# Optimization experiments

Hardware: AMD Instinct MI355X
Metric: run time of the kernel (lower is better)

The kernel has to match this reference:

```python
import jax, jax.numpy as jnp
import numpy as np

NUM_NODES = 15000


def _gcn_conv(x, W, b, src, dst, norm, num_nodes):
    # PyG GCNConv: x' = D^-1/2 (A + I) D^-1/2 (x W) + b
    h = x @ W                                   # [N, out]
    msg = h[src] * norm[:, None]                # gather + scale per edge
    out = jax.ops.segment_sum(msg, dst, num_segments=num_nodes)
    return out + b


def setup_inputs() -> dict:
    key = jax.random.key(0)
    ks = jax.random.split(key, 12)
    T = 100000
    E = 200000
    inp = {
        "x": jax.random.normal(ks[0], (NUM_NODES, 768), jnp.float32),
        "r_emb": jax.random.normal(ks[1], (T, 768), jnp.float32),
        "W1": jax.random.normal(ks[2], (768, 10), jnp.float32) * 0.05,
        "b1": jax.random.normal(ks[3], (10,), jnp.float32) * 0.05,
        "W2": jax.random.normal(ks[4], (10, 128), jnp.float32) * 0.05,
        "b2": jax.random.normal(ks[5], (128,), jnp.float32) * 0.05,
        "W_ih": jax.random.normal(ks[6], (512, 1024), jnp.float32) * 0.03,
        "W_hh": jax.random.normal(ks[7], (512, 128), jnp.float32) * 0.03,
        "b_ih": jax.random.normal(ks[8], (512,), jnp.float32) * 0.03,
        "b_hh": jax.random.normal(ks[9], (512,), jnp.float32) * 0.03,
        "edge_index": jax.random.randint(ks[10], (2, E), 0, NUM_NODES).astype(jnp.int64),
        "triples": jax.random.randint(ks[11], (T, 3), 0, NUM_NODES).astype(jnp.int64),
    }
    return inp


def reference(x, r_emb, W1, b1, W2, b2, W_ih, W_hh, b_ih, b_hh, edge_index, triples):
    N = x.shape[0]
    H = 128  # lstm hidden size
    # --- add self loops, symmetric GCN normalization ---
    loop = jnp.arange(N, dtype=edge_index.dtype)
    src = jnp.concatenate([edge_index[0], loop])
    dst = jnp.concatenate([edge_index[1], loop])
    deg = jax.ops.segment_sum(jnp.ones_like(dst, jnp.float32), dst, num_segments=N)
    dinv = jnp.where(deg > 0, jax.lax.rsqrt(deg), 0.0)
    norm = dinv[src] * dinv[dst]                      # [E+N]
    # --- 2-layer GCN ---
    h = jax.nn.relu(_gcn_conv(x, W1, b1, src, dst, norm, N))   # [N, 10]
    z = _gcn_conv(h, W2, b2, src, dst, norm, N)                # [N, 128]
    # --- per-triple LSTM scoring, batched (seq_len=1, zero init state) ---
    hvec = z[triples[:, 0]]                           # [T, 128]
    tvec = z[triples[:, 2]]                           # [T, 128]
    feat = jnp.concatenate([hvec, r_emb, tvec], axis=-1)       # [T, 1024]
    gates = feat @ W_ih.T + (b_ih + b_hh)             # [T, 512]; h0=0 so W_hh term vanishes
    i_g, f_g, g_g, o_g = jnp.split(gates, 4, axis=-1)  # torch gate order i,f,g,o
    c = jax.nn.sigmoid(i_g) * jnp.tanh(g_g)           # c0 = 0 -> forget term drops
    out = jax.nn.sigmoid(o_g) * jnp.tanh(c)           # [T, 128]
    score = jax.nn.sigmoid(jnp.sum(out, axis=-1))     # [T]
    return score
```

## Files before the change

kernel.cpp:

```cpp
#include <hip/hip_runtime.h>

#define NF 768
#define D1 10
#define D2 128
#define BM 64

typedef __attribute__((ext_vector_type(8))) short bf16x8;
typedef __attribute__((ext_vector_type(16))) float f32x16;

static __device__ __forceinline__ float sigf(float v){ return 1.0f/(1.0f+__expf(-v)); }
static __device__ __forceinline__ float tanhfast(float v){ return 2.0f/(1.0f+__expf(-2.0f*v)) - 1.0f; }
static __device__ __forceinline__ short f2bf(float f){
    unsigned u = __float_as_uint(f);
    u += 0x7fffu + ((u>>16)&1u);
    return (short)(u>>16);
}

static __device__ __forceinline__ void gload16(const void* g, void* l){
    __builtin_amdgcn_global_load_lds(
        (const __attribute__((address_space(1))) unsigned int*)(unsigned long long)g,
        (__attribute__((address_space(3))) unsigned int*)(unsigned long long)l,
        16, 0, 0);
}

static __device__ __forceinline__ short4 cvt4(float4 a){
    unsigned u0,u1;
    asm("v_cvt_pk_bf16_f32 %0, %1, %2" : "=v"(u0) : "v"(a.x), "v"(a.y));
    asm("v_cvt_pk_bf16_f32 %0, %1, %2" : "=v"(u1) : "v"(a.z), "v"(a.w));
    union { unsigned u[2]; short4 s; } r;
    r.u[0]=u0; r.u[1]=u1;
    return r.s;
}

__global__ void k_deg(const int* __restrict__ dst, int* __restrict__ cnt, int E){
    int e = blockIdx.x*256 + threadIdx.x;
    if(e<E) atomicAdd(&cnt[dst[e]], 1);
}

__global__ __launch_bounds__(256) void k_scan(const int* __restrict__ cnt,
                                              int* __restrict__ rowptr, int* __restrict__ rowcur,
                                              float* __restrict__ dinv, int N, int E){
    __shared__ int part[256];
    int t = threadIdx.x;
    int C = (N+255)/256;
    int lo = t*C, hi = lo+C; if(hi>N) hi=N; if(lo>N) lo=N;
    int s=0;
    for(int i=lo;i<hi;i++) s += cnt[i];
    part[t]=s;
    __syncthreads();
    if(t==0){
        int run=0;
        for(int i=0;i<256;i++){ int v=part[i]; part[i]=run; run+=v; }
        rowptr[N]=E;
    }
    __syncthreads();
    int run = part[t];
    for(int i=lo;i<hi;i++){
        rowptr[i]=run; rowcur[i]=run; run += cnt[i];
        dinv[i] = rsqrtf((float)cnt[i] + 1.0f);
    }
}

__global__ void k_fill(const int* __restrict__ src, const int* __restrict__ dst,
                       const float* __restrict__ dinv, int* __restrict__ rowcur,
                       int* __restrict__ esrc, float* __restrict__ enorm, int E){
    int e = blockIdx.x*256 + threadIdx.x;
    if(e>=E) return;
    int s=src[e], d=dst[e];
    int pos = atomicAdd(&rowcur[d], 1);
    esrc[pos]=s;
    enorm[pos]=dinv[s]*dinv[d];
}

__global__ __launch_bounds__(256) void k_h1(const float* __restrict__ x,
                                            const float* __restrict__ W1,
                                            float* __restrict__ h1, int N){
    __shared__ float wt[D1*NF];
    for(int idx=threadIdx.x; idx<NF*D1; idx+=256){
        int k=idx/D1, c=idx-k*D1;
        wt[c*NF+k]=W1[idx];
    }
    __syncthreads();
    int row = blockIdx.x*4 + (threadIdx.x>>6);
    int lane = threadIdx.x&63;
    if(row>=N) return;
    const float4* xr = (const float4*)(x + (size_t)row*NF);
    float acc[D1];
#pragma unroll
    for(int c=0;c<D1;c++) acc[c]=0.f;
#pragma unroll
    for(int i=0;i<3;i++){
        float4 v = xr[lane + 64*i];
#pragma unroll
        for(int c=0;c<D1;c++){
            float4 w = *(const float4*)&wt[c*NF + (lane+64*i)*4];
            acc[c] += v.x*w.x + v.y*w.y + v.z*w.z + v.w*w.w;
        }
    }
#pragma unroll
    for(int c=0;c<D1;c++){
        float v=acc[c];
#pragma unroll
        for(int off=32;off;off>>=1) v += __shfl_down(v,off,64);
        acc[c]=v;
    }
    if(lane==0){
#pragma unroll
        for(int c=0;c<D1;c++) h1[(size_t)row*D1+c]=acc[c];
    }
}

__global__ __launch_bounds__(128) void k_gh(const float* __restrict__ h1,
        const int* __restrict__ rowptr, const int* __restrict__ esrc,
        const float* __restrict__ enorm, const float* __restrict__ dinv,
        const float* __restrict__ b1, const float* __restrict__ W2,
        float* __restrict__ hz, int N){
    __shared__ float w2s[D1*D2];
    int tid = threadIdx.x;
    for(int i=tid;i<D1*D2;i+=128) w2s[i]=W2[i];
    __syncthreads();
    int node = blockIdx.x*2 + (tid>>6);
    int lane = tid&63;
    if(node>=N) return;
    int e0=rowptr[node], e1=rowptr[node+1];
    float acc[D1];
#pragma unroll
    for(int c=0;c<D1;c++) acc[c]=0.f;
    for(int e=e0+lane; e<e1; e+=64){
        int s=esrc[e]; float w=enorm[e];
        const float* hr = h1 + (size_t)s*D1;
#pragma unroll
        for(int c=0;c<D1;c++) acc[c] += hr[c]*w;
    }
#pragma unroll
    for(int c=0;c<D1;c++){
        float v=acc[c];
#pragma unroll
        for(int off=32;off;off>>=1) v += __shfl_down(v,off,64);
        acc[c] = __shfl(v, 0, 64);
    }
    float di=dinv[node], d2=di*di;
    const float* hr = h1 + (size_t)node*D1;
    float h[D1];
#pragma unroll
    for(int c=0;c<D1;c++){
        float v = acc[c] + hr[c]*d2 + b1[c];
        h[c] = v>0.f ? v : 0.f;
    }
    float o0=0.f, o1=0.f;
#pragma unroll
    for(int k=0;k<D1;k++){
        o0 += h[k]*w2s[k*D2 + lane];
        o1 += h[k]*w2s[k*D2 + 64 + lane];
    }
    hz[(size_t)node*D2 + lane]      = o0;
    hz[(size_t)node*D2 + 64 + lane] = o1;
}

__global__ __launch_bounds__(128) void k_gath2(const float* __restrict__ hz,
        const int* __restrict__ rowptr, const int* __restrict__ esrc,
        const float* __restrict__ enorm, const float* __restrict__ dinv,
        const float* __restrict__ b2, float* __restrict__ zbf, int N){
    int n = blockIdx.x;
    int c = threadIdx.x;
    int e0 = rowptr[n], e1 = rowptr[n+1];
    float di = dinv[n];
    float acc = hz[(size_t)n*D2+c]*di*di + b2[c];
    int e = e0;
    for(; e+1<e1; e+=2){
        int s0=esrc[e], s1=esrc[e+1];
        float w0=enorm[e], w1=enorm[e+1];
        acc += hz[(size_t)s0*D2+c]*w0 + hz[(size_t)s1*D2+c]*w1;
    }
    if(e<e1) acc += hz[(size_t)esrc[e]*D2+c]*enorm[e];
    zbf[(size_t)n*D2+c] = acc;
}

__global__ void k_wimgB(const float* __restrict__ Wih, ushort* __restrict__ img,
                        int* __restrict__ cnt, int N){
    int gid = blockIdx.x*256 + threadIdx.x;
    if(gid < N) cnt[gid] = 0;
    if(gid >= 12*64*64) return;
    int l = gid & 63;
    int ks16 = (gid>>6) & 63;
    int f = gid >> 12;
    int dd = l & 31, kb = l>>5;
    int wn = f/3, gi = f - wn*3;
    int gbase = (gi==0)?0:((gi==1)?256:384);
    int wrow = gbase + wn*32 + dd;
    int k = ks16*16 + kb*8;
    const float* p = Wih + (size_t)wrow*1024 + k;
    float4 v0=*(const float4*)p, v1=*(const float4*)(p+4);
    ushort o[8];
    o[0]=f2bf(v0.x); o[1]=f2bf(v0.y); o[2]=f2bf(v0.z); o[3]=f2bf(v0.w);
    o[4]=f2bf(v1.x); o[5]=f2bf(v1.y); o[6]=f2bf(v1.z); o[7]=f2bf(v1.w);
    *(int4*)(img + (size_t)gid*8) = *(int4*)o;
}

__global__ __launch_bounds__(256,3) void k_big(
    const float* __restrict__ remb, const ushort* __restrict__ img,
    const float* __restrict__ zbf, const float* __restrict__ b_ih,
    const float* __restrict__ b_hh, const int* __restrict__ trip,
    float* __restrict__ rowacc, int T)
{
    __shared__ ushort Ab[2][2*64*8];
    __shared__ ushort Br[3][12*512];
    int tid=threadIdx.x, lane=tid&63, w=tid>>6;
    int l31=lane&31, lh=lane>>5;
    int t0=blockIdx.x*BM;

    const int arow = w*16 + (lane>>2);
    const int asub = lane&3;
    int tc = t0 + arow; if(tc>=T) tc=T-1;
    const float* pzh = zbf + (size_t)trip[3*tc]*D2   + asub*4;
    const float* prm = remb + (size_t)tc*NF          + asub*4;
    const float* pzt = zbf + (size_t)trip[3*tc+2]*D2 + asub*4;
    const int awoff = ((asub>>1)*64 + arow)*8 + (asub&1)*4;
    const int ar0 = (lh*64 + l31)*8;
    const int ar1 = (lh*64 + 32 + l31)*8;

    f32x16 acc[2][3];
    const f32x16 zer = {0,0,0,0,0,0,0,0,0,0,0,0,0,0,0,0};
#pragma unroll
    for(int m=0;m<2;m++)
#pragma unroll
        for(int g=0;g<3;g++) acc[m][g]=zer;

    float4 pa[4];

#define ALOAD(C_) if((C_)<64){ \
    const float* s_; \
    if((C_)<8)       s_ = pzh + (C_)*16; \
    else if((C_)<56) s_ = prm + ((C_)-8)*16; \
    else             s_ = pzt + ((C_)-56)*16; \
    pa[(C_)&3] = *(const float4*)s_; }

#define AWRITE(C_) if((C_)<64){ \
    *(short4*)&Ab[(C_)&1][awoff] = cvt4(pa[(C_)&3]); }

#define BISSUE(C_) if((C_)<64){ \
    _Pragma("unroll") \
    for(int j_=0;j_<3;j_++){ \
        gload16(img + ((size_t)((w*3+j_)*64 + (C_))*64 + lane)*8, \
                &Br[(C_)%3][(w*3+j_)*512]); \
    } }

#define CH(C_,W_) { \
    asm volatile("s_waitcnt vmcnt(" W_ ")" ::: "memory"); \
    __builtin_amdgcn_sched_barrier(0); \
    asm volatile("s_waitcnt lgkmcnt(0)" ::: "memory"); \
    __builtin_amdgcn_s_barrier(); \
    __builtin_amdgcn_sched_barrier(0); \
    BISSUE((C_)+2) \
    __builtin_amdgcn_sched_barrier(0); \
    ALOAD((C_)+4) \
    __builtin_amdgcn_sched_barrier(0); \
    { \
        const ushort* a_ = &Ab[(C_)&1][0]; \
        const ushort* b_ = &Br[(C_)%3][0]; \
        bf16x8 A0_ = *(const bf16x8*)&a_[ar0]; \
        bf16x8 A1_ = *(const bf16x8*)&a_[ar1]; \
        bf16x8 B0_ = *(const bf16x8*)&b_[((w*3+0)*64+lane)*8]; \
        bf16x8 B1_ = *(const bf16x8*)&b_[((w*3+1)*64+lane)*8]; \
        bf16x8 B2_ = *(const bf16x8*)&b_[((w*3+2)*64+lane)*8]; \
        __builtin_amdgcn_s_setprio(1); \
        acc[0][0]=__builtin_amdgcn_mfma_f32_32x32x16_bf16(A0_,B0_,acc[0][0],0,0,0); \
        acc[0][1]=__builtin_amdgcn_mfma_f32_32x32x16_bf16(A0_,B1_,acc[0][1],0,0,0); \
        acc[0][2]=__builtin_amdgcn_mfma_f32_32x32x16_bf16(A0_,B2_,acc[0][2],0,0,0); \
        acc[1][0]=__builtin_amdgcn_mfma_f32_32x32x16_bf16(A1_,B0_,acc[1][0],0,0,0); \
        acc[1][1]=__builtin_amdgcn_mfma_f32_32x32x16_bf16(A1_,B1_,acc[1][1],0,0,0); \
        acc[1][2]=__builtin_amdgcn_mfma_f32_32x32x16_bf16(A1_,B2_,acc[1][2],0,0,0); \
        __builtin_amdgcn_s_setprio(0); \
    } \
    AWRITE((C_)+1) \
}

    ALOAD(0) ALOAD(1) ALOAD(2) ALOAD(3)
    __builtin_amdgcn_sched_barrier(0);
    BISSUE(0) BISSUE(1)
    __builtin_amdgcn_sched_barrier(0);
    AWRITE(0)

    CH(0 ,"3") CH(1 ,"4") CH(2 ,"5") CH(3 ,"5") CH(4 ,"5") CH(5 ,"5") CH(6 ,"5") CH(7 ,"5")
    CH(8 ,"5") CH(9 ,"5") CH(10,"5") CH(11,"5") CH(12,"5") CH(13,"5") CH(14,"5") CH(15,"5")
    CH(16,"5") CH(17,"5") CH(18,"5") CH(19,"5") CH(20,"5") CH(21,"5") CH(22,"5") CH(23,"5")
    CH(24,"5") CH(25,"5") CH(26,"5") CH(27,"5") CH(28,"5") CH(29,"5") CH(30,"5") CH(31,"5")
    CH(32,"5") CH(33,"5") CH(34,"5") CH(35,"5") CH(36,"5") CH(37,"5") CH(38,"5") CH(39,"5")
    CH(40,"5") CH(41,"5") CH(42,"5") CH(43,"5") CH(44,"5") CH(45,"5") CH(46,"5") CH(47,"5")
    CH(48,"5") CH(49,"5") CH(50,"5") CH(51,"5") CH(52,"5") CH(53,"5") CH(54,"5") CH(55,"5")
    CH(56,"5") CH(57,"5") CH(58,"5") CH(59,"5") CH(60,"5") CH(61,"4") CH(62,"3") CH(63,"0")
#undef CH
#undef BISSUE
#undef AWRITE
#undef ALOAD

    int d = w*32+l31;
    float bi=b_ih[d]+b_hh[d];
    float bg=b_ih[256+d]+b_hh[256+d];
    float bo=b_ih[384+d]+b_hh[384+d];
#pragma unroll
    for(int m=0;m<2;m++){
#pragma unroll
        for(int r=0;r<16;r++){
            int row = m*32 + (r&3)+8*(r>>2)+4*lh;
            int t = t0+row;
            float ov = 0.f;
            if(t<T){
                float ig = acc[m][0][r] + bi;
                float gg = acc[m][1][r] + bg;
                float og = acc[m][2][r] + bo;
                float cc = sigf(ig)*tanhfast(gg);
                ov = sigf(og)*tanhfast(cc);
            }
#pragma unroll
            for(int off=1; off<32; off<<=1) ov += __shfl_xor(ov, off, 64);
            if(l31==0 && t<T) atomicAdd(&rowacc[t], ov);
        }
    }
}

__global__ void k_sig(const float* __restrict__ rowacc, float* __restrict__ score, int T){
    int t = blockIdx.x*256 + threadIdx.x;
    if(t<T) score[t] = sigf(rowacc[t]);
}

extern "C" void kernel_launch(void* const* d_in, const int* in_sizes, int n_in,
                              void* d_out, int out_size, void* d_ws, size_t ws_size,
                              hipStream_t stream){
    const float* x    = (const float*)d_in[0];
    const float* remb = (const float*)d_in[1];
    const float* W1   = (const float*)d_in[2];
    const float* b1   = (const float*)d_in[3];
    const float* W2   = (const float*)d_in[4];
    const float* b2   = (const float*)d_in[5];
    const float* Wih  = (const float*)d_in[6];
    const float* b_ih = (const float*)d_in[8];
    const float* b_hh = (const float*)d_in[9];
    const int*   ei   = (const int*)d_in[10];
    const int*   trip = (const int*)d_in[11];
    float* score = (float*)d_out;

    const int N = in_sizes[0]/NF;
    const int E = in_sizes[10]/2;
    const int T = in_sizes[11]/3;
    const int* src = ei;
    const int* dst = ei + E;

    float* ws = (float*)d_ws;
    size_t o = 0;
    ushort* img  = (ushort*)(ws+o); o += (size_t)12*64*64*8/2;
    float* zbf   = ws+o;            o += (size_t)N*D2;
    float* rowacc= ws+o;            o += (size_t)((T+7)&~7);
    int*   cnt    = (int*)(ws+o);   o += (size_t)((N+8)&~7);
    int*   rowptr = (int*)(ws+o);   o += (size_t)((N+8)&~7);
    int*   rowcur = (int*)(ws+o);   o += (size_t)((N+8)&~7);
    int*   esrc   = (int*)(ws+o);   o += (size_t)E;
    float* enorm  = ws+o;           o += (size_t)E;
    float* dinv   = ws+o;           o += (size_t)((N+7)&~7);
    float* h1     = ws+o;           o += (size_t)N*D1;
    float* hz     = ws+o;           o += (size_t)N*D2;
    (void)ws_size; (void)n_in; (void)out_size;

    hipMemsetAsync(rowacc, 0, (size_t)T*sizeof(float), stream);

    k_wimgB<<<dim3((12*64*64+255)/256), dim3(256), 0, stream>>>(Wih, img, cnt, N);
    k_deg  <<<dim3((E+255)/256), dim3(256), 0, stream>>>(dst, cnt, E);
    k_scan <<<dim3(1), dim3(256), 0, stream>>>(cnt, rowptr, rowcur, dinv, N, E);
    k_fill <<<dim3((E+255)/256), dim3(256), 0, stream>>>(src, dst, dinv, rowcur, esrc, enorm, E);
    k_h1   <<<dim3((N+3)/4), dim3(256), 0, stream>>>(x, W1, h1, N);
    k_gh   <<<dim3((N+1)/2), dim3(128), 0, stream>>>(h1, rowptr, esrc, enorm, dinv, b1, W2, hz, N);
    k_gath2<<<dim3(N), dim3(128), 0, stream>>>(hz, rowptr, esrc, enorm, dinv, b2, zbf, N);
    k_big  <<<dim3((T+BM-1)/BM), dim3(256), 0, stream>>>(remb, img, zbf, b_ih, b_hh, trip, rowacc, T);
    k_sig  <<<dim3((T+255)/256), dim3(256), 0, stream>>>(rowacc, score, T);
}
```

Before: 306.4 us.

## Precompute per-node z·W_ih projections and shrink main GEMM K to r_emb only

The head and tail node embedding parts of the LSTM input projection are computed once per node (N=15000) by a new MFMA kernel. Results go into a bf16 table of size N×768, and the per-triple GEMM is reduced to the 768-wide r_emb segment. The main kernel now adds the gathered per-node gate contributions in the epilogue instead of doing the z columns in the K loop, and its pipeline is rebuilt with 32-wide K steps and double buffering. This removes redundant per-triple work on node features (T=100k vs N=15k). The cost is an extra kernel, extra bf16 rounding of the projected values, and scattered gathers in the epilogue.

Result: slower. 367.9 us (+20.1%).

```diff
diff --git a/kernel.cpp b/kernel.cpp
--- a/kernel.cpp
+++ b/kernel.cpp
@@ -14,6 +14,9 @@
     unsigned u = __float_as_uint(f);
     u += 0x7fffu + ((u>>16)&1u);
     return (short)(u>>16);
+}
+static __device__ __forceinline__ float bf2f(ushort h){
+    return __uint_as_float(((unsigned)h)<<16);
 }
 
 static __device__ __forceinline__ void gload16(const void* g, void* l){
@@ -180,16 +183,16 @@
                         int* __restrict__ cnt, int N){
     int gid = blockIdx.x*256 + threadIdx.x;
     if(gid < N) cnt[gid] = 0;
-    if(gid >= 12*64*64) return;
+    if(gid >= 12*48*64) return;
     int l = gid & 63;
-    int ks16 = (gid>>6) & 63;
-    int f = gid >> 12;
+    int ks16 = (gid>>6) % 48;
+    int f = gid / (48*64);
     int dd = l & 31, kb = l>>5;
     int wn = f/3, gi = f - wn*3;
     int gbase = (gi==0)?0:((gi==1)?256:384);
     int wrow = gbase + wn*32 + dd;
     int k = ks16*16 + kb*8;
-    const float* p = Wih + (size_t)wrow*1024 + k;
+    const float* p = Wih + (size_t)wrow*1024 + 128 + k;
     float4 v0=*(const float4*)p, v1=*(const float4*)(p+4);
     ushort o[8];
     o[0]=f2bf(v0.x); o[1]=f2bf(v0.y); o[2]=f2bf(v0.z); o[3]=f2bf(v0.w);
@@ -197,27 +200,99 @@
     *(int4*)(img + (size_t)gid*8) = *(int4*)o;
 }
 
-__global__ __launch_bounds__(256,3) void k_big(
+__global__ void k_wimgZ(const float* __restrict__ Wih, ushort* __restrict__ img){
+    int gid = blockIdx.x*256 + threadIdx.x;
+    if(gid >= 24*8*64) return;
+    int l = gid & 63;
+    int ks16 = (gid>>6) & 7;
+    int f = gid >> 9;
+    int j = f*32 + (l&31);
+    int kb = l>>5;
+    int k = ks16*16 + kb*8;
+    int jq = (j<384)? j : j-384;
+    int wrow = (jq<128)? jq : jq+128;
+    int wcol = (j<384)? k : (896+k);
+    const float* p = Wih + (size_t)wrow*1024 + wcol;
+    float4 v0=*(const float4*)p, v1=*(const float4*)(p+4);
+    ushort o[8];
+    o[0]=f2bf(v0.x); o[1]=f2bf(v0.y); o[2]=f2bf(v0.z); o[3]=f2bf(v0.w);
+    o[4]=f2bf(v1.x); o[5]=f2bf(v1.y); o[6]=f2bf(v1.z); o[7]=f2bf(v1.w);
+    *(int4*)(img + (size_t)gid*8) = *(int4*)o;
+}
+
+__global__ __launch_bounds__(256) void k_zw_m(const float* __restrict__ z,
+                                              const ushort* __restrict__ img,
+                                              ushort* __restrict__ zwht, int N){
+    __shared__ ushort As[8*64*8];
+    int tid=threadIdx.x, lane=tid&63, w=tid>>6;
+    int n0 = blockIdx.x*32;
+#pragma unroll
+    for(int i=0;i<2;i++){
+        int s = tid + 256*i;
+        int ks16 = s>>6, l = s&63;
+        int row = l&31, kb=l>>5;
+        int n = n0+row; if(n>=N) n=N-1;
+        const float* p = z + (size_t)n*D2 + ks16*16 + kb*8;
+        float4 v0=*(const float4*)p, v1=*(const float4*)(p+4);
+        ushort o[8];
+        o[0]=f2bf(v0.x); o[1]=f2bf(v0.y); o[2]=f2bf(v0.z); o[3]=f2bf(v0.w);
+        o[4]=f2bf(v1.x); o[5]=f2bf(v1.y); o[6]=f2bf(v1.z); o[7]=f2bf(v1.w);
+        *(int4*)(&As[(size_t)s*8]) = *(int4*)o;
+    }
+    __syncthreads();
+    f32x16 acc[6];
+    const f32x16 zer = {0,0,0,0,0,0,0,0,0,0,0,0,0,0,0,0};
+#pragma unroll
+    for(int nf=0;nf<6;nf++) acc[nf]=zer;
+#pragma unroll
+    for(int ks16=0;ks16<8;ks16++){
+        bf16x8 a = *(const bf16x8*)&As[(ks16*64+lane)*8];
+#pragma unroll
+        for(int nf=0;nf<6;nf++){
+            int f = w*6+nf;
+            bf16x8 b = *(const bf16x8*)(img + ((size_t)(f*8+ks16)*64 + lane)*8);
+            acc[nf] = __builtin_amdgcn_mfma_f32_32x32x16_bf16(a,b,acc[nf],0,0,0);
+        }
+    }
+    int l31=lane&31, lh=lane>>5;
+#pragma unroll
+    for(int nf=0;nf<6;nf++){
+        int j = (w*6+nf)*32 + l31;
+#pragma unroll
+        for(int r=0;r<16;r++){
+            int row = (r&3)+8*(r>>2)+4*lh;
+            int n = n0+row;
+            if(n<N) zwht[(size_t)n*768 + j] = (ushort)f2bf(acc[nf][r]);
+        }
+    }
+}
+
+__global__ __launch_bounds__(256,2) void k_big(
     const float* __restrict__ remb, const ushort* __restrict__ img,
-    const float* __restrict__ zbf, const float* __restrict__ b_ih,
+    const ushort* __restrict__ zwht, const float* __restrict__ b_ih,
     const float* __restrict__ b_hh, const int* __restrict__ trip,
     float* __restrict__ rowacc, int T)
 {
-    __shared__ ushort Ab[2][2*64*8];
-    __shared__ ushort Br[3][12*512];
+    __shared__ ushort Ab[2][4*64*8];
+    __shared__ ushort Br[2][24*512];
+    __shared__ int sh_th[BM], sh_tt[BM];
     int tid=threadIdx.x, lane=tid&63, w=tid>>6;
     int l31=lane&31, lh=lane>>5;
     int t0=blockIdx.x*BM;
 
+    if(tid<BM){
+        int t=t0+tid, tc=(t<T)?t:T-1;
+        sh_th[tid]=trip[3*tc]; sh_tt[tid]=trip[3*tc+2];
+    }
+
     const int arow = w*16 + (lane>>2);
     const int asub = lane&3;
     int tc = t0 + arow; if(tc>=T) tc=T-1;
-    const float* pzh = zbf + (size_t)trip[3*tc]*D2   + asub*4;
-    const float* prm = remb + (size_t)tc*NF          + asub*4;
-    const float* pzt = zbf + (size_t)trip[3*tc+2]*D2 + asub*4;
-    const int awoff = ((asub>>1)*64 + arow)*8 + (asub&1)*4;
-    const int ar0 = (lh*64 + l31)*8;
-    const int ar1 = (lh*64 + 32 + l31)*8;
+    const float* prm = remb + (size_t)tc*NF + asub*4;
+    const int aw0 = ((0*2 + (asub>>1))*64 + arow)*8 + (asub&1)*4;
+    const int aw1 = ((1*2 + (asub>>1))*64 + arow)*8 + (asub&1)*4;
+    const int ar00 = ((0*2+lh)*64 + l31)*8,      ar01 = ((0*2+lh)*64 + 32 + l31)*8;
+    const int ar10 = ((1*2+lh)*64 + l31)*8,      ar11 = ((1*2+lh)*64 + 32 + l31)*8;
 
     f32x16 acc[2][3];
     const f32x16 zer = {0,0,0,0,0,0,0,0,0,0,0,0,0,0,0,0};
@@ -226,23 +301,22 @@
 #pragma unroll
         for(int g=0;g<3;g++) acc[m][g]=zer;
 
-    float4 pa[4];
-
-#define ALOAD(C_) if((C_)<64){ \
-    const float* s_; \
-    if((C_)<8)       s_ = pzh + (C_)*16; \
-    else if((C_)<56) s_ = prm + ((C_)-8)*16; \
-    else             s_ = pzt + ((C_)-56)*16; \
-    pa[(C_)&3] = *(const float4*)s_; }
-
-#define AWRITE(C_) if((C_)<64){ \
-    *(short4*)&Ab[(C_)&1][awoff] = cvt4(pa[(C_)&3]); }
-
-#define BISSUE(C_) if((C_)<64){ \
+    float4 pa[2][2];
+
+#define ALOAD(C_) if((C_)<24){ \
+    pa[(C_)&1][0] = *(const float4*)(prm + (C_)*32); \
+    pa[(C_)&1][1] = *(const float4*)(prm + (C_)*32 + 16); }
+
+#define AWRITE(C_) if((C_)<24){ \
+    *(short4*)&Ab[(C_)&1][aw0] = cvt4(pa[(C_)&1][0]); \
+    *(short4*)&Ab[(C_)&1][aw1] = cvt4(pa[(C_)&1][1]); }
+
+#define BISSUE(C_) if((C_)<24){ \
     _Pragma("unroll") \
-    for(int j_=0;j_<3;j_++){ \
-        gload16(img + ((size_t)((w*3+j_)*64 + (C_))*64 + lane)*8, \
-                &Br[(C_)%3][(w*3+j_)*512]); \
+    for(int j_=0;j_<6;j_++){ \
+        int f_ = w*3 + (j_>>1), s_ = j_&1; \
+        gload16(img + ((size_t)(f_*48 + (C_)*2 + s_)*64 + lane)*8, \
+                &Br[(C_)&1][(f_*2+s_)*512]); \
     } }
 
 #define CH(C_,W_) { \
@@ -251,44 +325,53 @@
     asm volatile("s_waitcnt lgkmcnt(0)" ::: "memory"); \
     __builtin_amdgcn_s_barrier(); \
     __builtin_amdgcn_sched_barrier(0); \
-    BISSUE((C_)+2) \
-    __builtin_amdgcn_sched_barrier(0); \
-    ALOAD((C_)+4) \
+    BISSUE((C_)+1) \
+    ALOAD((C_)+2) \
     __builtin_amdgcn_sched_barrier(0); \
     { \
         const ushort* a_ = &Ab[(C_)&1][0]; \
-        const ushort* b_ = &Br[(C_)%3][0]; \
-        bf16x8 A0_ = *(const bf16x8*)&a_[ar0]; \
-        bf16x8 A1_ = *(const bf16x8*)&a_[ar1]; \
-        bf16x8 B0_ = *(const bf16x8*)&b_[((w*3+0)*64+lane)*8]; \
-        bf16x8 B1_ = *(const bf16x8*)&b_[((w*3+1)*64+lane)*8]; \
-        bf16x8 B2_ = *(const bf16x8*)&b_[((w*3+2)*64+lane)*8]; \
+        const ushort* b_ = &Br[(C_)&1][0]; \
+        bf16x8 A00 = *(const bf16x8*)&a_[ar00]; \
+        bf16x8 A01 = *(const bf16x8*)&a_[ar01]; \
+        bf16x8 B00 = *(const bf16x8*)&b_[((w*3+0)*2+0)*512 + lane*8]; \
+        bf16x8 B01 = *(const bf16x8*)&b_[((w*3+1)*2+0)*512 + lane*8]; \
+        bf16x8 B02 = *(const bf16x8*)&b_[((w*3+2)*2+0)*512 + lane*8]; \
         __builtin_amdgcn_s_setprio(1); \
-        acc[0][0]=__builtin_amdgcn_mfma_f32_32x32x16_bf16(A0_,B0_,acc[0][0],0,0,0); \
-        acc[0][1]=__builtin_amdgcn_mfma_f32_32x32x16_bf16(A0_,B1_,acc[0][1],0,0,0); \
-        acc[0][2]=__builtin_amdgcn_mfma_f32_32x32x16_bf16(A0_,B2_,acc[0][2],0,0,0); \
-        acc[1][0]=__builtin_amdgcn_mfma_f32_32x32x16_bf16(A1_,B0_,acc[1][0],0,0,0); \
-        acc[1][1]=__builtin_amdgcn_mfma_f32_32x32x16_bf16(A1_,B1_,acc[1][1],0,0,0); \
-        acc[1][2]=__builtin_amdgcn_mfma_f32_32x32x16_bf16(A1_,B2_,acc[1][2],0,0,0); \
+        acc[0][0]=__builtin_amdgcn_mfma_f32_32x32x16_bf16(A00,B00,acc[0][0],0,0,0); \
+        acc[0][1]=__builtin_amdgcn_mfma_f32_32x32x16_bf16(A00,B01,acc[0][1],0,0,0); \
+        acc[0][2]=__builtin_amdgcn_mfma_f32_32x32x16_bf16(A00,B02,acc[0][2],0,0,0); \
+        acc[1][0]=__builtin_amdgcn_mfma_f32_32x32x16_bf16(A01,B00,acc[1][0],0,0,0); \
+        acc[1][1]=__builtin_amdgcn_mfma_f32_32x32x16_bf16(A01,B01,acc[1][1],0,0,0); \
+        acc[1][2]=__builtin_amdgcn_mfma_f32_32x32x16_bf16(A01,B02,acc[1][2],0,0,0); \
+        __builtin_amdgcn_s_setprio(0); \
+        bf16x8 A10 = *(const bf16x8*)&a_[ar10]; \
+        bf16x8 A11 = *(const bf16x8*)&a_[ar11]; \
+        bf16x8 B10 = *(const bf16x8*)&b_[((w*3+0)*2+1)*512 + lane*8]; \
+        bf16x8 B11 = *(const bf16x8*)&b_[((w*3+1)*2+1)*512 + lane*8]; \
+        bf16x8 B12 = *(const bf16x8*)&b_[((w*3+2)*2+1)*512 + lane*8]; \
+        __builtin_amdgcn_s_setprio(1); \
+        acc[0][0]=__builtin_amdgcn_mfma_f32_32x32x16_bf16(A10,B10,acc[0][0],0,0,0); \
+        acc[0][1]=__builtin_amdgcn_mfma_f32_32x32x16_bf16(A10,B11,acc[0][1],0,0,0); \
+        acc[0][2]=__builtin_amdgcn_mfma_f32_32x32x16_bf16(A10,B12,acc[0][2],0,0,0); \
+        acc[1][0]=__builtin_amdgcn_mfma_f32_32x32x16_bf16(A11,B10,acc[1][0],0,0,0); \
+        acc[1][1]=__builtin_amdgcn_mfma_f32_32x32x16_bf16(A11,B11,acc[1][1],0,0,0); \
+        acc[1][2]=__builtin_amdgcn_mfma_f32_32x32x16_bf16(A11,B12,acc[1][2],0,0,0); \
         __builtin_amdgcn_s_setprio(0); \
     } \
     AWRITE((C_)+1) \
 }
 
-    ALOAD(0) ALOAD(1) ALOAD(2) ALOAD(3)
+    ALOAD(0)
     __builtin_amdgcn_sched_barrier(0);
-    BISSUE(0) BISSUE(1)
+    BISSUE(0)
+    ALOAD(1)
     __builtin_amdgcn_sched_barrier(0);
     AWRITE(0)
 
-    CH(0 ,"3") CH(1 ,"4") CH(2 ,"5") CH(3 ,"5") CH(4 ,"5") CH(5 ,"5") CH(6 ,"5") CH(7 ,"5")
-    CH(8 ,"5") CH(9 ,"5") CH(10,"5") CH(11,"5") CH(12,"5") CH(13,"5") CH(14,"5") CH(15,"5")
-    CH(16,"5") CH(17,"5") CH(18,"5") CH(19,"5") CH(20,"5") CH(21,"5") CH(22,"5") CH(23,"5")
-    CH(24,"5") CH(25,"5") CH(26,"5") CH(27,"5") CH(28,"5") CH(29,"5") CH(30,"5") CH(31,"5")
-    CH(32,"5") CH(33,"5") CH(34,"5") CH(35,"5") CH(36,"5") CH(37,"5") CH(38,"5") CH(39,"5")
-    CH(40,"5") CH(41,"5") CH(42,"5") CH(43,"5") CH(44,"5") CH(45,"5") CH(46,"5") CH(47,"5")
-    CH(48,"5") CH(49,"5") CH(50,"5") CH(51,"5") CH(52,"5") CH(53,"5") CH(54,"5") CH(55,"5")
-    CH(56,"5") CH(57,"5") CH(58,"5") CH(59,"5") CH(60,"5") CH(61,"4") CH(62,"3") CH(63,"0")
+    CH(0 ,"2") CH(1 ,"2") CH(2 ,"2") CH(3 ,"2") CH(4 ,"2") CH(5 ,"2")
+    CH(6 ,"2") CH(7 ,"2") CH(8 ,"2") CH(9 ,"2") CH(10,"2") CH(11,"2")
+    CH(12,"2") CH(13,"2") CH(14,"2") CH(15,"2") CH(16,"2") CH(17,"2")
+    CH(18,"2") CH(19,"2") CH(20,"2") CH(21,"2") CH(22,"2") CH(23,"0")
 #undef CH
 #undef BISSUE
 #undef AWRITE
@@ -306,9 +389,11 @@
             int t = t0+row;
             float ov = 0.f;
             if(t<T){
-                float ig = acc[m][0][r] + bi;
-                float gg = acc[m][1][r] + bg;
-                float og = acc[m][2][r] + bo;
+                const ushort* zh = zwht + (size_t)sh_th[row]*768;
+                const ushort* zt = zwht + (size_t)sh_tt[row]*768 + 384;
+                float ig = acc[m][0][r] + bf2f(zh[d])     + bf2f(zt[d])     + bi;
+                float gg = acc[m][1][r] + bf2f(zh[128+d]) + bf2f(zt[128+d]) + bg;
+                float og = acc[m][2][r] + bf2f(zh[256+d]) + bf2f(zt[256+d]) + bo;
                 float cc = sigf(ig)*tanhfast(gg);
                 ov = sigf(og)*tanhfast(cc);
             }
@@ -348,28 +433,32 @@
 
     float* ws = (float*)d_ws;
     size_t o = 0;
-    ushort* img  = (ushort*)(ws+o); o += (size_t)12*64*64*8/2;
-    float* zbf   = ws+o;            o += (size_t)N*D2;
-    float* rowacc= ws+o;            o += (size_t)((T+7)&~7);
-    int*   cnt    = (int*)(ws+o);   o += (size_t)((N+8)&~7);
-    int*   rowptr = (int*)(ws+o);   o += (size_t)((N+8)&~7);
-    int*   rowcur = (int*)(ws+o);   o += (size_t)((N+8)&~7);
-    int*   esrc   = (int*)(ws+o);   o += (size_t)E;
-    float* enorm  = ws+o;           o += (size_t)E;
-    float* dinv   = ws+o;           o += (size_t)((N+7)&~7);
-    float* h1     = ws+o;           o += (size_t)N*D1;
-    float* hz     = ws+o;           o += (size_t)N*D2;
+    ushort* img   = (ushort*)(ws+o); o += (size_t)12*48*64*8/2;
+    ushort* imgZ  = (ushort*)(ws+o); o += (size_t)24*8*64*8/2;
+    ushort* zwht  = (ushort*)(ws+o); o += (size_t)N*768/2;
+    float* zbf    = ws+o;            o += (size_t)N*D2;
+    float* rowacc = ws+o;            o += (size_t)((T+7)&~7);
+    int*   cnt    = (int*)(ws+o);    o += (size_t)((N+8)&~7);
+    int*   rowptr = (int*)(ws+o);    o += (size_t)((N+8)&~7);
+    int*   rowcur = (int*)(ws+o);    o += (size_t)((N+8)&~7);
+    int*   esrc   = (int*)(ws+o);    o += (size_t)E;
+    float* enorm  = ws+o;            o += (size_t)E;
+    float* dinv   = ws+o;            o += (size_t)((N+7)&~7);
+    float* h1     = ws+o;            o += (size_t)N*D1;
+    float* hz     = ws+o;            o += (size_t)N*D2;
     (void)ws_size; (void)n_in; (void)out_size;
 
     hipMemsetAsync(rowacc, 0, (size_t)T*sizeof(float), stream);
 
-    k_wimgB<<<dim3((12*64*64+255)/256), dim3(256), 0, stream>>>(Wih, img, cnt, N);
+    k_wimgB<<<dim3((12*48*64+255)/256), dim3(256), 0, stream>>>(Wih, img, cnt, N);
+    k_wimgZ<<<dim3((24*8*64+255)/256),  dim3(256), 0, stream>>>(Wih, imgZ);
     k_deg  <<<dim3((E+255)/256), dim3(256), 0, stream>>>(dst, cnt, E);
     k_scan <<<dim3(1), dim3(256), 0, stream>>>(cnt, rowptr, rowcur, dinv, N, E);
     k_fill <<<dim3((E+255)/256), dim3(256), 0, stream>>>(src, dst, dinv, rowcur, esrc, enorm, E);
     k_h1   <<<dim3((N+3)/4), dim3(256), 0, stream>>>(x, W1, h1, N);
     k_gh   <<<dim3((N+1)/2), dim3(128), 0, stream>>>(h1, rowptr, esrc, enorm, dinv, b1, W2, hz, N);
     k_gath2<<<dim3(N), dim3(128), 0, stream>>>(hz, rowptr, esrc, enorm, dinv, b2, zbf, N);
-    k_big  <<<dim3((T+BM-1)/BM), dim3(256), 0, stream>>>(remb, img, zbf, b_ih, b_hh, trip, rowacc, T);
+    k_zw_m <<<dim3((N+31)/32), dim3(256), 0, stream>>>(zbf, imgZ, zwht, N);
+    k_big  <<<dim3((T+BM-1)/BM), dim3(256), 0, stream>>>(remb, img, zwht, b_ih, b_hh, trip, rowacc, T);
     k_sig  <<<dim3((T+255)/256), dim3(256), 0, stream>>>(rowacc, score, T);
 }
```

## Load W_ih B-fragments directly into registers instead of staging through LDS

Applied to the files above, without the earlier changes.

The main LSTM-gate GEMM kernel no longer stages the bf16 weight image through shared memory with async global-to-LDS copies. Each wave now loads its B fragments straight into registers, double-buffered one chunk ahead. The A buffer becomes triple-buffered so the A write can move before the barrier. This cuts LDS traffic and the vmcnt bookkeeping, but adds register pressure, so launch bounds drop from 3 to 2 blocks per SU, which lowers occupancy and leaves less time to hide global-load latency.

Measured after the change: 306.6 us. About the same (+0.1%).

```diff
diff --git a/kernel.cpp b/kernel.cpp
--- a/kernel.cpp
+++ b/kernel.cpp
@@ -14,13 +14,6 @@
     unsigned u = __float_as_uint(f);
     u += 0x7fffu + ((u>>16)&1u);
     return (short)(u>>16);
-}
-
-static __device__ __forceinline__ void gload16(const void* g, void* l){
-    __builtin_amdgcn_global_load_lds(
-        (const __attribute__((address_space(1))) unsigned int*)(unsigned long long)g,
-        (__attribute__((address_space(3))) unsigned int*)(unsigned long long)l,
-        16, 0, 0);
 }
 
 static __device__ __forceinline__ short4 cvt4(float4 a){
@@ -197,14 +190,13 @@
     *(int4*)(img + (size_t)gid*8) = *(int4*)o;
 }
 
-__global__ __launch_bounds__(256,3) void k_big(
+__global__ __launch_bounds__(256,2) void k_big(
     const float* __restrict__ remb, const ushort* __restrict__ img,
     const float* __restrict__ zbf, const float* __restrict__ b_ih,
     const float* __restrict__ b_hh, const int* __restrict__ trip,
     float* __restrict__ rowacc, int T)
 {
-    __shared__ ushort Ab[2][2*64*8];
-    __shared__ ushort Br[3][12*512];
+    __shared__ ushort Ab[3][2*64*8];
     int tid=threadIdx.x, lane=tid&63, w=tid>>6;
     int l31=lane&31, lh=lane>>5;
     int t0=blockIdx.x*BM;
@@ -219,6 +211,10 @@
     const int ar0 = (lh*64 + l31)*8;
     const int ar1 = (lh*64 + 32 + l31)*8;
 
+    const ushort* wb0 = img + ((size_t)((w*3+0)*64)*64 + lane)*8;
+    const ushort* wb1 = img + ((size_t)((w*3+1)*64)*64 + lane)*8;
+    const ushort* wb2 = img + ((size_t)((w*3+2)*64)*64 + lane)*8;
+
     f32x16 acc[2][3];
     const f32x16 zer = {0,0,0,0,0,0,0,0,0,0,0,0,0,0,0,0};
 #pragma unroll
@@ -227,6 +223,7 @@
         for(int g=0;g<3;g++) acc[m][g]=zer;
 
     float4 pa[4];
+    bf16x8 qb[2][3];
 
 #define ALOAD(C_) if((C_)<64){ \
     const float* s_; \
@@ -236,33 +233,28 @@
     pa[(C_)&3] = *(const float4*)s_; }
 
 #define AWRITE(C_) if((C_)<64){ \
-    *(short4*)&Ab[(C_)&1][awoff] = cvt4(pa[(C_)&3]); }
-
-#define BISSUE(C_) if((C_)<64){ \
-    _Pragma("unroll") \
-    for(int j_=0;j_<3;j_++){ \
-        gload16(img + ((size_t)((w*3+j_)*64 + (C_))*64 + lane)*8, \
-                &Br[(C_)%3][(w*3+j_)*512]); \
-    } }
-
-#define CH(C_,W_) { \
-    asm volatile("s_waitcnt vmcnt(" W_ ")" ::: "memory"); \
+    *(short4*)&Ab[(C_)%3][awoff] = cvt4(pa[(C_)&3]); }
+
+#define BLOAD(C_) if((C_)<64){ \
+    qb[(C_)&1][0] = *(const bf16x8*)(wb0 + (size_t)(C_)*512); \
+    qb[(C_)&1][1] = *(const bf16x8*)(wb1 + (size_t)(C_)*512); \
+    qb[(C_)&1][2] = *(const bf16x8*)(wb2 + (size_t)(C_)*512); }
+
+#define CH(C_) { \
+    BLOAD((C_)+1) \
+    ALOAD((C_)+4) \
     __builtin_amdgcn_sched_barrier(0); \
+    AWRITE((C_)+1) \
     asm volatile("s_waitcnt lgkmcnt(0)" ::: "memory"); \
     __builtin_amdgcn_s_barrier(); \
     __builtin_amdgcn_sched_barrier(0); \
-    BISSUE((C_)+2) \
-    __builtin_amdgcn_sched_barrier(0); \
-    ALOAD((C_)+4) \
-    __builtin_amdgcn_sched_barrier(0); \
     { \
-        const ushort* a_ = &Ab[(C_)&1][0]; \
-        const ushort* b_ = &Br[(C_)%3][0]; \
+        const ushort* a_ = &Ab[(C_)%3][0]; \
         bf16x8 A0_ = *(const bf16x8*)&a_[ar0]; \
         bf16x8 A1_ = *(const bf16x8*)&a_[ar1]; \
-        bf16x8 B0_ = *(const bf16x8*)&b_[((w*3+0)*64+lane)*8]; \
-        bf16x8 B1_ = *(const bf16x8*)&b_[((w*3+1)*64+lane)*8]; \
-        bf16x8 B2_ = *(const bf16x8*)&b_[((w*3+2)*64+lane)*8]; \
+        bf16x8 B0_ = qb[(C_)&1][0]; \
+        bf16x8 B1_ = qb[(C_)&1][1]; \
+        bf16x8 B2_ = qb[(C_)&1][2]; \
         __builtin_amdgcn_s_setprio(1); \
         acc[0][0]=__builtin_amdgcn_mfma_f32_32x32x16_bf16(A0_,B0_,acc[0][0],0,0,0); \
         acc[0][1]=__builtin_amdgcn_mfma_f32_32x32x16_bf16(A0_,B1_,acc[0][1],0,0,0); \
@@ -272,25 +264,24 @@
         acc[1][2]=__builtin_amdgcn_mfma_f32_32x32x16_bf16(A1_,B2_,acc[1][2],0,0,0); \
         __builtin_amdgcn_s_setprio(0); \
     } \
-    AWRITE((C_)+1) \
 }
 
     ALOAD(0) ALOAD(1) ALOAD(2) ALOAD(3)
     __builtin_amdgcn_sched_barrier(0);
-    BISSUE(0) BISSUE(1)
+    BLOAD(0)
     __builtin_amdgcn_sched_barrier(0);
     AWRITE(0)
 
-    CH(0 ,"3") CH(1 ,"4") CH(2 ,"5") CH(3 ,"5") CH(4 ,"5") CH(5 ,"5") CH(6 ,"5") CH(7 ,"5")
-    CH(8 ,"5") CH(9 ,"5") CH(10,"5") CH(11,"5") CH(12,"5") CH(13,"5") CH(14,"5") CH(15,"5")
-    CH(16,"5") CH(17,"5") CH(18,"5") CH(19,"5") CH(20,"5") CH(21,"5") CH(22,"5") CH(23,"5")
-    CH(24,"5") CH(25,"5") CH(26,"5") CH(27,"5") CH(28,"5") CH(29,"5") CH(30,"5") CH(31,"5")
-    CH(32,"5") CH(33,"5") CH(34,"5") CH(35,"5") CH(36,"5") CH(37,"5") CH(38,"5") CH(39,"5")
-    CH(40,"5") CH(41,"5") CH(42,"5") CH(43,"5") CH(44,"5") CH(45,"5") CH(46,"5") CH(47,"5")
-    CH(48,"5") CH(49,"5") CH(50,"5") CH(51,"5") CH(52,"5") CH(53,"5") CH(54,"5") CH(55,"5")
-    CH(56,"5") CH(57,"5") CH(58,"5") CH(59,"5") CH(60,"5") CH(61,"4") CH(62,"3") CH(63,"0")
+    CH(0)  CH(1)  CH(2)  CH(3)  CH(4)  CH(5)  CH(6)  CH(7)
+    CH(8)  CH(9)  CH(10) CH(11) CH(12) CH(13) CH(14) CH(15)
+    CH(16) CH(17) CH(18) CH(19) CH(20) CH(21) CH(22) CH(23)
+    CH(24) CH(25) CH(26) CH(27) CH(28) CH(29) CH(30) CH(31)
+    CH(32) CH(33) CH(34) CH(35) CH(36) CH(37) CH(38) CH(39)
+    CH(40) CH(41) CH(42) CH(43) CH(44) CH(45) CH(46) CH(47)
+    CH(48) CH(49) CH(50) CH(51) CH(52) CH(53) CH(54) CH(55)
+    CH(56) CH(57) CH(58) CH(59) CH(60) CH(61) CH(62) CH(63)
 #undef CH
-#undef BISSUE
+#undef BLOAD
 #undef AWRITE
 #undef ALOAD
 
@@ -348,17 +339,17 @@
 
     float* ws = (float*)d_ws;
     size_t o = 0;
-    ushort* img  = (ushort*)(ws+o); o += (size_t)12*64*64*8/2;
-    float* zbf   = ws+o;            o += (size_t)N*D2;
-    float* rowacc= ws+o;            o += (size_t)((T+7)&~7);
-    int*   cnt    = (int*)(ws+o);   o += (size_t)((N+8)&~7);
-    int*   rowptr = (int*)(ws+o);   o += (size_t)((N+8)&~7);
-    int*   rowcur = (int*)(ws+o);   o += (size_t)((N+8)&~7);
-    int*   esrc   = (int*)(ws+o);   o += (size_t)E;
-    float* enorm  = ws+o;           o += (size_t)E;
-    float* dinv   = ws+o;           o += (size_t)((N+7)&~7);
-    float* h1     = ws+o;           o += (size_t)N*D1;
-    float* hz     = ws+o;           o += (size_t)N*D2;
+    ushort* img   = (ushort*)(ws+o); o += (size_t)12*64*64*8/2;
+    float* zbf    = ws+o;            o += (size_t)N*D2;
+    float* rowacc = ws+o;            o += (size_t)((T+7)&~7);
+    int*   cnt    = (int*)(ws+o);    o += (size_t)((N+8)&~7);
+    int*   rowptr = (int*)(ws+o);    o += (size_t)((N+8)&~7);
+    int*   rowcur = (int*)(ws+o);    o += (size_t)((N+8)&~7);
+    int*   esrc   = (int*)(ws+o);    o += (size_t)E;
+    float* enorm  = ws+o;            o += (size_t)E;
+    float* dinv   = ws+o;            o += (size_t)((N+7)&~7);
+    float* h1     = ws+o;            o += (size_t)N*D1;
+    float* hz     = ws+o;            o += (size_t)N*D2;
     (void)ws_size; (void)n_in; (void)out_size;
 
     hipMemsetAsync(rowacc, 0, (size_t)T*sizeof(float), stream);
```
